# Performance work log

Hardware: AMD Instinct MI355X
Metric: run time of the kernel (lower is better)

## Reference

```python
import jax, jax.numpy as jnp
import numpy as np

HID = 100  # LSTM hidden size (fixed in module)


def _lstm_final(x, Wih, Whh, bih, bhh, reverse):
    # x: [N, T, Hin]; returns final hidden state [N, HID] (PyTorch gate order i,f,g,o)
    xs = jnp.flip(x, axis=1) if reverse else x
    pre = jnp.einsum('nth,gh->ntg', xs, Wih) + bih + bhh  # [N, T, 4*HID]
    N = x.shape[0]
    h0 = jnp.zeros((N, HID), x.dtype)
    c0 = jnp.zeros((N, HID), x.dtype)

    def step(carry, pt):
        h, c = carry
        g = pt + h @ Whh.T
        i, f, gg, o = jnp.split(g, 4, axis=-1)
        c = jax.nn.sigmoid(f) * c + jax.nn.sigmoid(i) * jnp.tanh(gg)
        h = jax.nn.sigmoid(o) * jnp.tanh(c)
        return (h, c), None

    (h, c), _ = jax.lax.scan(step, (h0, c0), jnp.swapaxes(pre, 0, 1))
    return h


def setup_inputs():
    key = jax.random.key(0)
    ks = jax.random.split(key, 16)
    H, B, S, NP, PL = 768, 40, 128, 100, 20
    w = lambda k, shape: jax.random.normal(k, shape, jnp.float32) * 0.02
    return {
        'bert_output': jax.random.normal(ks[0], (B, S, H), jnp.float32),
        'commonsense': jax.random.normal(ks[1], (B * NP, PL, H), jnp.float32),
        'attention_mask': jnp.ones((B, S), jnp.int32),
        'commonsense_mask': jnp.ones((B, NP), jnp.int32),
        'b_size': 8, 'num_cand': 5, 'num_path': NP, 'path_len': PL,
        'lstm_Wih_f': w(ks[2], (4 * HID, H)), 'lstm_Whh_f': w(ks[3], (4 * HID, HID)),
        'lstm_bih_f': jnp.zeros((4 * HID,), jnp.float32), 'lstm_bhh_f': jnp.zeros((4 * HID,), jnp.float32),
        'lstm_Wih_b': w(ks[4], (4 * HID, H)), 'lstm_Whh_b': w(ks[5], (4 * HID, HID)),
        'lstm_bih_b': jnp.zeros((4 * HID,), jnp.float32), 'lstm_bhh_b': jnp.zeros((4 * HID,), jnp.float32),
        'proj_W': w(ks[6], (H, 2 * HID)), 'proj_b': jnp.zeros((H,), jnp.float32),
        'W1_w': w(ks[7], (1, H)), 'W1_b': jnp.zeros((1,), jnp.float32),
        'W2_w': w(ks[8], (1, H)), 'W2_b': jnp.zeros((1,), jnp.float32),
        'W3': w(ks[9], (1, 1, H)),
        'attp_W': w(ks[10], (H, 4 * H)), 'attp_b': jnp.zeros((H,), jnp.float32),
        'ln_w': jnp.ones((H,), jnp.float32), 'ln_b': jnp.zeros((H,), jnp.float32),
    }


def reference(bert_output, commonsense, attention_mask, commonsense_mask,
              b_size, num_cand, num_path, path_len,
              lstm_Wih_f, lstm_Whh_f, lstm_bih_f, lstm_bhh_f,
              lstm_Wih_b, lstm_Whh_b, lstm_bih_b, lstm_bhh_b,
              proj_W, proj_b, W1_w, W1_b, W2_w, W2_b, W3,
              attp_W, attp_b, ln_w, ln_b):
    Bc = b_size * num_cand
    # bidirectional LSTM over commonsense paths; only final hidden states are used
    h_f = _lstm_final(commonsense, lstm_Wih_f, lstm_Whh_f, lstm_bih_f, lstm_bhh_f, False)
    h_b = _lstm_final(commonsense, lstm_Wih_b, lstm_Whh_b, lstm_bih_b, lstm_bhh_b, True)
    enc = jnp.concatenate([h_f, h_b], axis=-1)               # [Bc*NP, 200]
    cs = jax.nn.relu(enc @ proj_W.T + proj_b).reshape(Bc, num_path, -1)  # [B, P, H]
    # trilinear BiDAF-style scores
    part1 = bert_output @ W1_w.T + W1_b                      # [B, S, 1]
    part2 = (cs @ W2_w.T + W2_b).transpose(0, 2, 1)          # [B, 1, P]
    part3 = jnp.einsum('bsh,bph->bsp', W3 * bert_output, cs)  # [B, S, P]
    mask_cs = (1.0 - commonsense_mask.astype(jnp.float32)) * -10000.0
    mask_dqa = (1.0 - attention_mask.astype(jnp.float32)) * -10000.0
    total = part1 + part2 + part3 + mask_cs[:, None, :] + mask_dqa[:, :, None]
    cs_att = jax.nn.softmax(total, axis=-1)                  # over paths
    weight_cs = jnp.einsum('bsp,bph->bsh', cs_att, cs)
    ctx_att = jax.nn.softmax(total, axis=1)                  # over context tokens
    probs = jnp.einsum('bsp,btp->bst', cs_att, ctx_att)      # [B, S, S]
    weighted_context = jnp.einsum('bst,bth->bsh', probs, bert_output)
    cat = jnp.concatenate([bert_output, weight_cs, bert_output * weight_cs,
                           bert_output * weighted_context], axis=-1)
    x = jax.nn.relu(cat @ attp_W.T + attp_b) + bert_output
    u = x.mean(-1, keepdims=True)
    s = ((x - u) ** 2).mean(-1, keepdims=True)
    return ln_w * ((x - u) / jnp.sqrt(s + 1e-12)) + ln_b
```

## Files before the change

### kernel.cpp

```cpp
#include <hip/hip_runtime.h>


typedef unsigned short ushort_t;
typedef unsigned int u32;
typedef __attribute__((ext_vector_type(8))) short short8;
typedef __attribute__((ext_vector_type(4))) float f32x4;
typedef __attribute__((address_space(1))) const u32 gu32;
typedef __attribute__((address_space(3))) u32 lu32;

__device__ __forceinline__ ushort_t f2bf(float f) {
  u32 x = __builtin_bit_cast(u32, f);
  u32 r = (x + 0x7fffu + ((x >> 16) & 1u)) >> 16;
  return (ushort_t)r;
}
__device__ __forceinline__ float bflo(u32 u) { return __builtin_bit_cast(float, u << 16); }
__device__ __forceinline__ float bfhi(u32 u) { return __builtin_bit_cast(float, u & 0xffff0000u); }
__device__ __forceinline__ u32 cvtpk(float lo, float hi) {
  u32 r;
  asm("v_cvt_pk_bf16_f32 %0, %1, %2" : "=v"(r) : "v"(lo), "v"(hi));
  return r;
}

__device__ __forceinline__ float sigm(float x) { return 1.f / (1.f + __expf(-x)); }
__device__ __forceinline__ float tanh_f(float x) { return 1.f - 2.f / (__expf(2.f * x) + 1.f); }


__global__ void prep_weights(const float* __restrict__ Wih_f, const float* __restrict__ Wih_b,
                             const float* __restrict__ Whh_f, const float* __restrict__ Whh_b,
                             const float* __restrict__ bih_f, const float* __restrict__ bhh_f,
                             const float* __restrict__ bih_b, const float* __restrict__ bhh_b,
                             const float* __restrict__ projW, const float* __restrict__ attpW,
                             ushort_t* __restrict__ wihcat, ushort_t* __restrict__ whhcat,
                             float* __restrict__ biascat, ushort_t* __restrict__ projw_bf,
                             ushort_t* __restrict__ attpw_bf) {
  const int TOT = 614400 + 102400 + 800 + 196608 + 2359296;
  for (int idx = blockIdx.x * 256 + threadIdx.x; idx < TOT; idx += gridDim.x * 256) {
    if (idx < 614400) {
      int g = idx / 768, k = idx % 768;
      float v = g < 400 ? Wih_f[g * 768 + k] : Wih_b[(g - 400) * 768 + k];
      wihcat[idx] = f2bf(v);
    } else if (idx < 716800) {
      int e = idx - 614400; int g = e / 128, j = e % 128;
      float v = 0.f;
      if (j < 100) v = g < 400 ? Whh_f[g * 100 + j] : Whh_b[(g - 400) * 100 + j];
      whhcat[e] = f2bf(v);
    } else if (idx < 717600) {
      int g = idx - 716800;
      biascat[g] = g < 400 ? bih_f[g] + bhh_f[g] : bih_b[g - 400] + bhh_b[g - 400];
    } else if (idx < 914208) {
      int e = idx - 717600; int o = e / 256, j = e % 256;
      float v = 0.f;
      if (j < 100) v = projW[o * 200 + j];
      else if (j >= 128 && j < 228) v = projW[o * 200 + 100 + (j - 128)];
      projw_bf[e] = f2bf(v);
    } else {
      int e = idx - 914208;
      attpw_bf[e] = f2bf(attpW[e]);
    }
  }
}

__global__ void convert_x_t(const float4* __restrict__ x4, ushort_t* __restrict__ xb) {
  for (int i = blockIdx.x * 256 + threadIdx.x; i < 15360000; i += gridDim.x * 256) {
    int seq = i / 3840;
    int rem = i - seq * 3840;
    int t = rem / 192;
    int k4 = rem - t * 192;
    float4 v = x4[i];
    ushort4 o;
    o.x = f2bf(v.x); o.y = f2bf(v.y); o.z = f2bf(v.z); o.w = f2bf(v.w);
    *reinterpret_cast<ushort4*>(&xb[((size_t)t * 4000 + seq) * 768 + k4 * 4]) = o;
  }
}

__global__ __launch_bounds__(256) void prep_bert(const float* __restrict__ bert,
                                                 const float* __restrict__ W3,
                                                 ushort_t* __restrict__ bw3,
                                                 ushort_t* __restrict__ bT) {
  __shared__ ushort_t tl[64 * 130];
  int ht = blockIdx.x, b = blockIdx.y;
  int h0 = ht * 64, tid = threadIdx.x;
  for (int e = tid; e < 8192; e += 256) {
    int t = e >> 6, hh = e & 63;
    float v = bert[((size_t)b * 128 + t) * 768 + h0 + hh];
    bw3[((size_t)b * 128 + t) * 768 + h0 + hh] = f2bf(v * W3[h0 + hh]);
    tl[hh * 130 + t] = f2bf(v);
  }
  __syncthreads();
  for (int e = tid; e < 8192; e += 256) {
    int hh = e >> 7, t = e & 127;
    bT[((size_t)b * 768 + h0 + hh) * 128 + t] = tl[hh * 130 + t];
  }
}

__global__ __launch_bounds__(256) void csT_k(const ushort_t* __restrict__ csb,
                                             ushort_t* __restrict__ csT) {
  __shared__ ushort_t tl[64 * 130];
  int ht = blockIdx.x, b = blockIdx.y;
  int h0 = ht * 64, tid = threadIdx.x;
  for (int e = tid; e < 6400; e += 256) {
    int p = e >> 6, hh = e & 63;
    tl[hh * 130 + p] = csb[((size_t)b * 100 + p) * 768 + h0 + hh];
  }
  __syncthreads();
  for (int e = tid; e < 8192; e += 256) {
    int hh = e >> 7, p = e & 127;
    csT[((size_t)b * 768 + h0 + hh) * 128 + p] = (p < 100) ? tl[hh * 130 + p] : (ushort_t)0;
  }
}


template <int EPI>
__global__ __launch_bounds__(256) void gemm128(
    const ushort_t* __restrict__ A, int lda,
    const ushort_t* __restrict__ B, int ldb,
    int M, int N, int KT,
    const float* __restrict__ bias,
    const float* __restrict__ resid,
    float* __restrict__ C, int ldc,
    ushort_t* __restrict__ C2,
    int nbn, int swq, int swr)
{
  __shared__ __align__(16) ushort_t lsA[128 * 64];
  __shared__ __align__(16) ushort_t lsB[128 * 64];
  int bm, bn;
  if (nbn > 0) {
    int bid = blockIdx.x, xcd = bid & 7, slot = bid >> 3;
    int L = (xcd < swr) ? xcd * (swq + 1) + slot
                        : swr * (swq + 1) + (xcd - swr) * swq + slot;
    bm = L / nbn; bn = L - bm * nbn;
  } else {
    bm = blockIdx.x; bn = blockIdx.y;
  }
  int m0 = bm * 128, n0 = bn * 128;
  int tid = threadIdx.x, lane = tid & 63, w = tid >> 6;
  int wr = w >> 1, wc = w & 1;
  int l15 = lane & 15, lk = lane >> 4;
  f32x4 acc[4][4];
  #pragma unroll
  for (int i = 0; i < 4; ++i)
    #pragma unroll
    for (int j = 0; j < 4; ++j)
      #pragma unroll
      for (int r = 0; r < 4; ++r) acc[i][j][r] = 0.f;

  int r_in = lane >> 3, p = lane & 7;
  for (int kt = 0; kt < KT; ++kt) {
    __syncthreads();
    #pragma unroll
    for (int i = 0; i < 4; ++i) {
      int seg = w * 4 + i;
      int row = seg * 8 + r_in;
      int sl = p ^ (row & 7);
      int m = m0 + row;
      if (m < M)
        __builtin_amdgcn_global_load_lds(
            (gu32*)(A + (size_t)m * lda + kt * 64 + sl * 8),
            (lu32*)(lsA + seg * 512), 16, 0, 0);
      int n = n0 + row;
      if (n < N)
        __builtin_amdgcn_global_load_lds(
            (gu32*)(B + (size_t)n * ldb + kt * 64 + sl * 8),
            (lu32*)(lsB + seg * 512), 16, 0, 0);
    }
    __syncthreads();
    #pragma unroll
    for (int ks = 0; ks < 2; ++ks) {
      short8 af[4], bfv[4];
      #pragma unroll
      for (int f = 0; f < 4; ++f) {
        int row = wr * 64 + f * 16 + l15;
        af[f] = *reinterpret_cast<const short8*>(
            &lsA[row * 64 + (((ks * 4 + lk) ^ (row & 7)) << 3)]);
        int rowb = wc * 64 + f * 16 + l15;
        bfv[f] = *reinterpret_cast<const short8*>(
            &lsB[rowb * 64 + (((ks * 4 + lk) ^ (rowb & 7)) << 3)]);
      }
      #pragma unroll
      for (int fm = 0; fm < 4; ++fm)
        #pragma unroll
        for (int fn = 0; fn < 4; ++fn)
          acc[fm][fn] = __builtin_amdgcn_mfma_f32_16x16x32_bf16(af[fm], bfv[fn], acc[fm][fn], 0, 0, 0);
    }
  }
  if (EPI == 0) {
    ushort_t* P = (ushort_t*)C;
    #pragma unroll
    for (int fm = 0; fm < 4; ++fm) {
      int mb = m0 + wr * 64 + fm * 16;
      int t = mb / 4000;
      int sq = mb - t * 4000;
      int cch = sq >> 4;
      #pragma unroll
      for (int fn = 0; fn < 4; ++fn) {
        int nb = n0 + wc * 64 + fn * 16;
        if (nb < N) {
          int nl = nb < 400 ? nb : nb - 400;
          int nq = (nb < 400 ? 0 : 25) + (nl >> 4);
          float bsv = bias[nb + l15];
          uint2 pk;
          pk.x = cvtpk(acc[fm][fn][0] + bsv, acc[fm][fn][1] + bsv);
          pk.y = cvtpk(acc[fm][fn][2] + bsv, acc[fm][fn][3] + bsv);
          *reinterpret_cast<uint2*>(
              &P[((((size_t)t * 250 + cch) * 50 + nq) << 8) + l15 * 16 + lk * 4]) = pk;
        }
      }
    }
  } else {
    #pragma unroll
    for (int fm = 0; fm < 4; ++fm)
      #pragma unroll
      for (int fn = 0; fn < 4; ++fn)
        #pragma unroll
        for (int r = 0; r < 4; ++r) {
          int m = m0 + wr * 64 + fm * 16 + lk * 4 + r;
          int n = n0 + wc * 64 + fn * 16 + l15;
          if (m < M && n < N) {
            float v = acc[fm][fn][r] + bias[n];
            v = fmaxf(v, 0.f);
            if (EPI == 2) v += resid[(size_t)m * ldc + n];
            C[(size_t)m * ldc + n] = v;
            if (EPI == 1 && C2) C2[(size_t)m * ldc + n] = f2bf(v);
          }
        }
  }
}


template <int EPI>
__global__ __launch_bounds__(256) void gemm128b(
    const ushort_t* __restrict__ A, long long sA, int lda,
    const ushort_t* __restrict__ Bm, long long sB, int ldb,
    int M, int N, int KT,
    float* __restrict__ Cf, ushort_t* __restrict__ Cb, long long sC, int ldc,
    const float* __restrict__ p1, const float* __restrict__ p2,
    const int* __restrict__ am, const int* __restrict__ cm)
{
  __shared__ __align__(16) ushort_t lsA[128 * 64];
  __shared__ __align__(16) ushort_t lsB[128 * 64];
  int b = blockIdx.z;
  const ushort_t* Ab = A + (size_t)b * sA;
  const ushort_t* Bb = Bm + (size_t)b * sB;
  int n0 = blockIdx.x * 128;
  int tid = threadIdx.x, lane = tid & 63, w = tid >> 6;
  int wr = w >> 1, wc = w & 1;
  int l15 = lane & 15, lk = lane >> 4;
  f32x4 acc[4][4];
  #pragma unroll
  for (int i = 0; i < 4; ++i)
    #pragma unroll
    for (int j = 0; j < 4; ++j)
      #pragma unroll
      for (int r = 0; r < 4; ++r) acc[i][j][r] = 0.f;

  int r_in = lane >> 3, p = lane & 7;
  for (int kt = 0; kt < KT; ++kt) {
    __syncthreads();
    #pragma unroll
    for (int i = 0; i < 4; ++i) {
      int seg = w * 4 + i;
      int row = seg * 8 + r_in;
      int sl = p ^ (row & 7);
      if (row < M)
        __builtin_amdgcn_global_load_lds(
            (gu32*)(Ab + (size_t)row * lda + kt * 64 + sl * 8),
            (lu32*)(lsA + seg * 512), 16, 0, 0);
      int n = n0 + row;
      if (n < N)
        __builtin_amdgcn_global_load_lds(
            (gu32*)(Bb + (size_t)n * ldb + kt * 64 + sl * 8),
            (lu32*)(lsB + seg * 512), 16, 0, 0);
    }
    __syncthreads();
    #pragma unroll
    for (int ks = 0; ks < 2; ++ks) {
      short8 af[4], bfv[4];
      #pragma unroll
      for (int f = 0; f < 4; ++f) {
        int row = wr * 64 + f * 16 + l15;
        af[f] = *reinterpret_cast<const short8*>(
            &lsA[row * 64 + (((ks * 4 + lk) ^ (row & 7)) << 3)]);
        int rowb = wc * 64 + f * 16 + l15;
        bfv[f] = *reinterpret_cast<const short8*>(
            &lsB[rowb * 64 + (((ks * 4 + lk) ^ (rowb & 7)) << 3)]);
      }
      #pragma unroll
      for (int fm = 0; fm < 4; ++fm)
        #pragma unroll
        for (int fn = 0; fn < 4; ++fn)
          acc[fm][fn] = __builtin_amdgcn_mfma_f32_16x16x32_bf16(af[fm], bfv[fn], acc[fm][fn], 0, 0, 0);
    }
  }
  #pragma unroll
  for (int fm = 0; fm < 4; ++fm)
    #pragma unroll
    for (int fn = 0; fn < 4; ++fn)
      #pragma unroll
      for (int r = 0; r < 4; ++r) {
        int m = wr * 64 + fm * 16 + lk * 4 + r;
        int n = n0 + wc * 64 + fn * 16 + l15;
        if (m < M && n < N) {
          float v = acc[fm][fn][r];
          if (EPI == 10) {
            v += p1[b * M + m] + p2[b * N + n];
            v += (1.f - (float)am[b * M + m]) * -10000.f;
            v += (1.f - (float)cm[b * N + n]) * -10000.f;
            Cf[(size_t)b * sC + (size_t)m * ldc + n] = v;
          } else {
            Cb[(size_t)b * sC + (size_t)m * ldc + n] = f2bf(v);
          }
        }
      }
}


__global__ __launch_bounds__(256) void lstm_recur(
    const ushort_t* __restrict__ pre,
    const ushort_t* __restrict__ whh,
    ushort_t* __restrict__ hcat)
{
  __shared__ __align__(16) ushort_t gx[25 * 256];
  __shared__ __align__(16) ushort_t h_lds[16 * 128];

  int dir = blockIdx.y;
  int c = blockIdx.x;
  int tid = threadIdx.x, lane = tid & 63, w = tid >> 6;
  int s = lane & 15, lk = lane >> 4;

  short8 wf[7][4];
  #pragma unroll
  for (int qi = 0; qi < 7; ++qi) {
    int q = w + qi * 4;
    if (q < 25) {
      const ushort_t* wp = whh + ((size_t)dir * 400 + q * 16 + s) * 128;
      #pragma unroll
      for (int ks = 0; ks < 4; ++ks)
        wf[qi][ks] = *reinterpret_cast<const short8*>(wp + ks * 32 + lk * 8);
    }
  }
  for (int e = tid; e < 1024; e += 256)
    *reinterpret_cast<u32*>(&h_lds[e * 2]) = 0u;

  float cst[2][4];
  #pragma unroll
  for (int g = 0; g < 2; ++g)
    #pragma unroll
    for (int r = 0; r < 4; ++r) cst[g][r] = 0.f;

  uint2 pvA[7], pvB[7];
  {
    int tt0 = dir ? 19 : 0;
    const ushort_t* pb = pre + ((((size_t)tt0 * 250 + c) * 50 + dir * 25) << 8);
    #pragma unroll
    for (int qi = 0; qi < 7; ++qi) {
      int q = w + qi * 4;
      if (q < 25) pvA[qi] = *reinterpret_cast<const uint2*>(pb + (q << 8) + s * 16 + lk * 4);
    }
  }
  __syncthreads();

  auto step = [&](uint2 (&pvc)[7], uint2 (&pvn)[7], int t) {
    f32x4 acc[7];
    #pragma unroll
    for (int qi = 0; qi < 7; ++qi)
      #pragma unroll
      for (int r = 0; r < 4; ++r) acc[qi][r] = 0.f;
    #pragma unroll
    for (int ks = 0; ks < 4; ++ks) {
      short8 af = *reinterpret_cast<const short8*>(
          &h_lds[s * 128 + (((ks * 4 + lk) ^ s) << 3)]);
      #pragma unroll
      for (int qi = 0; qi < 7; ++qi)
        if (w + qi * 4 < 25)
          acc[qi] = __builtin_amdgcn_mfma_f32_16x16x32_bf16(af, wf[qi][ks], acc[qi], 0, 0, 0);
    }
    #pragma unroll
    for (int qi = 0; qi < 7; ++qi)
      if (w + qi * 4 < 25) {
        acc[qi][0] += bflo(pvc[qi].x); acc[qi][1] += bfhi(pvc[qi].x);
        acc[qi][2] += bflo(pvc[qi].y); acc[qi][3] += bfhi(pvc[qi].y);
      }
    if (t + 1 < 20) {
      int tn = dir ? 19 - (t + 1) : (t + 1);
      const ushort_t* pb = pre + ((((size_t)tn * 250 + c) * 50 + dir * 25) << 8);
      #pragma unroll
      for (int qi = 0; qi < 7; ++qi) {
        int q = w + qi * 4;
        if (q < 25) pvn[qi] = *reinterpret_cast<const uint2*>(pb + (q << 8) + s * 16 + lk * 4);
      }
    }
    #pragma unroll
    for (int qi = 0; qi < 7; ++qi) {
      int q = w + qi * 4;
      if (q < 25) {
        ushort4 pk;
        pk.x = f2bf(acc[qi][0]); pk.y = f2bf(acc[qi][1]);
        pk.z = f2bf(acc[qi][2]); pk.w = f2bf(acc[qi][3]);
        *reinterpret_cast<ushort4*>(&gx[(q << 8) + s * 16 + lk * 4]) = pk;
      }
    }
    __syncthreads();
    #pragma unroll
    for (int gd = 0; gd < 2; ++gd) {
      int gi = w + gd * 4;
      if (gi < 7) {
        int j = gi * 16 + s;
        if (j < 100) {
          auto ld2 = [&](int q, int sp) {
            return *reinterpret_cast<const uint2*>(&gx[(q << 8) + sp * 16 + lk * 4]);
          };
          uint2 iv = ld2(gi, s);
          uint2 fv = (s < 12) ? ld2(6 + gi, s + 4) : ld2(7 + gi, s - 12);
          uint2 gv = (s < 8) ? ld2(12 + gi, s + 8) : ld2(13 + gi, s - 8);
          uint2 ov = (s < 4) ? ld2(18 + gi, s + 12) : ld2(19 + gi, s - 4);
          float ia[4] = {bflo(iv.x), bfhi(iv.x), bflo(iv.y), bfhi(iv.y)};
          float fa[4] = {bflo(fv.x), bfhi(fv.x), bflo(fv.y), bfhi(fv.y)};
          float ga[4] = {bflo(gv.x), bfhi(gv.x), bflo(gv.y), bfhi(gv.y)};
          float oa[4] = {bflo(ov.x), bfhi(ov.x), bflo(ov.y), bfhi(ov.y)};
          #pragma unroll
          for (int r = 0; r < 4; ++r) {
            float cc = sigm(fa[r]) * cst[gd][r] + sigm(ia[r]) * tanh_f(ga[r]);
            cst[gd][r] = cc;
            int row = lk * 4 + r;
            h_lds[row * 128 + (((j >> 3) ^ row) << 3) + (j & 7)] =
                f2bf(sigm(oa[r]) * tanh_f(cc));
          }
        }
      }
    }
    __syncthreads();
  };

  #pragma unroll 1
  for (int tp = 0; tp < 10; ++tp) {
    step(pvA, pvB, 2 * tp);
    step(pvB, pvA, 2 * tp + 1);
  }

  {
    int row = tid >> 4, sl = tid & 15;
    uint2 v = *reinterpret_cast<const uint2*>(&h_lds[row * 128 + ((sl ^ row) << 3)]);
    *reinterpret_cast<uint2*>(&hcat[(size_t)(c * 16 + row) * 256 + dir * 128 + sl * 8]) = v;
  }
}


__global__ void rowdot(const float* __restrict__ X, int ld, const float* __restrict__ w,
                       const float* __restrict__ b0, float* __restrict__ out, int nrows) {
  int row = blockIdx.x;
  if (row >= nrows) return;
  int lane = threadIdx.x;
  const float* x = X + (size_t)row * ld;
  float s = 0.f;
  for (int k = lane; k < 768; k += 64) s += x[k] * w[k];
  for (int off = 32; off; off >>= 1) s += __shfl_down(s, off);
  if (lane == 0) out[row] = s + b0[0];
}

__global__ void softmax_both(const float* __restrict__ total,
                             ushort_t* __restrict__ csatt,
                             ushort_t* __restrict__ ctxatt) {
  int bid = blockIdx.x;
  int lane = threadIdx.x;
  if (bid < 5120) {
    const float* x = total + (size_t)bid * 100;
    float e0 = x[lane];
    bool has1 = (lane + 64) < 100;
    float e1 = has1 ? x[lane + 64] : -3.4e38f;
    float m = fmaxf(e0, e1);
    for (int off = 32; off; off >>= 1) m = fmaxf(m, __shfl_xor(m, off));
    float s0 = expf(e0 - m), s1 = has1 ? expf(e1 - m) : 0.f;
    float s = s0 + s1;
    for (int off = 32; off; off >>= 1) s += __shfl_xor(s, off);
    float inv = 1.f / s;
    csatt[(size_t)bid * 128 + lane] = f2bf(s0 * inv);
    csatt[(size_t)bid * 128 + lane + 64] = has1 ? f2bf(s1 * inv) : (ushort_t)0;
  } else {
    int idx = bid - 5120;
    int b = idx / 100, p = idx - b * 100;
    const float* base = total + (size_t)b * 12800 + p;
    float e0 = base[lane * 100], e1 = base[(lane + 64) * 100];
    float m = fmaxf(e0, e1);
    for (int off = 32; off; off >>= 1) m = fmaxf(m, __shfl_xor(m, off));
    float s0 = expf(e0 - m), s1 = expf(e1 - m);
    float s = s0 + s1;
    for (int off = 32; off; off >>= 1) s += __shfl_xor(s, off);
    float inv = 1.f / s;
    ctxatt[((size_t)b * 128 + lane) * 128 + p] = f2bf(s0 * inv);
    ctxatt[((size_t)b * 128 + lane + 64) * 128 + p] = f2bf(s1 * inv);
  }
}

__global__ void catk(const float* __restrict__ bert, const ushort_t* __restrict__ wcs,
                     const ushort_t* __restrict__ wctx, ushort_t* __restrict__ cat) {
  const int TOT = 5120 * 3072;
  for (int i = blockIdx.x * 256 + threadIdx.x; i < TOT; i += gridDim.x * 256) {
    int row = i / 3072, col = i - row * 3072;
    int seg = col / 768;
    int h = col - seg * 768;
    size_t e = (size_t)row * 768 + h;
    ushort_t o;
    if (seg == 0) o = f2bf(bert[e]);
    else if (seg == 1) o = wcs[e];
    else if (seg == 2) o = f2bf(bert[e] * bflo((u32)wcs[e]));
    else o = f2bf(bert[e] * bflo((u32)wctx[e]));
    cat[i] = o;
  }
}

__global__ __launch_bounds__(256) void layernorm(float* __restrict__ X,
                                                 const float* __restrict__ w,
                                                 const float* __restrict__ bta) {
  int row = blockIdx.x;
  float* x = X + (size_t)row * 768;
  int t = threadIdx.x;
  float v[3];
  float s = 0.f;
  #pragma unroll
  for (int i = 0; i < 3; ++i) { v[i] = x[t + 256 * i]; s += v[i]; }
  __shared__ float red[256];
  red[t] = s; __syncthreads();
  for (int off = 128; off; off >>= 1) { if (t < off) red[t] += red[t + off]; __syncthreads(); }
  float mean = red[0] * (1.f / 768.f);
  __syncthreads();
  float q = 0.f;
  #pragma unroll
  for (int i = 0; i < 3; ++i) { float d = v[i] - mean; q += d * d; }
  red[t] = q; __syncthreads();
  for (int off = 128; off; off >>= 1) { if (t < off) red[t] += red[t + off]; __syncthreads(); }
  float inv = rsqrtf(red[0] * (1.f / 768.f) + 1e-12f);
  #pragma unroll
  for (int i = 0; i < 3; ++i) {
    int k = t + 256 * i;
    x[k] = w[k] * ((v[i] - mean) * inv) + bta[k];
  }
}


extern "C" void kernel_launch(void* const* d_in, const int* in_sizes, int n_in,
                              void* d_out, int out_size, void* d_ws, size_t ws_size,
                              hipStream_t stream) {
  (void)in_sizes; (void)n_in; (void)out_size; (void)ws_size;
  const float* bert  = (const float*)d_in[0];
  const float* cmn   = (const float*)d_in[1];
  const int*   amask = (const int*)d_in[2];
  const int*   cmask = (const int*)d_in[3];
  const float* Wih_f = (const float*)d_in[8];
  const float* Whh_f = (const float*)d_in[9];
  const float* bih_f = (const float*)d_in[10];
  const float* bhh_f = (const float*)d_in[11];
  const float* Wih_b = (const float*)d_in[12];
  const float* Whh_b = (const float*)d_in[13];
  const float* bih_b = (const float*)d_in[14];
  const float* bhh_b = (const float*)d_in[15];
  const float* projW = (const float*)d_in[16];
  const float* projb = (const float*)d_in[17];
  const float* W1w   = (const float*)d_in[18];
  const float* W1b   = (const float*)d_in[19];
  const float* W2w   = (const float*)d_in[20];
  const float* W2b   = (const float*)d_in[21];
  const float* W3    = (const float*)d_in[22];
  const float* attpW = (const float*)d_in[23];
  const float* attpb = (const float*)d_in[24];
  const float* lnw   = (const float*)d_in[25];
  const float* lnb   = (const float*)d_in[26];

  char* base = (char*)d_ws;
  size_t off = 0;
  auto alloc = [&](size_t bytes) -> char* {
    char* r = base + off;
    off += (bytes + 255) & ~(size_t)255;
    return r;
  };
  ushort_t* wihcat   = (ushort_t*)alloc(800 * 768 * 2);
  ushort_t* whhcat   = (ushort_t*)alloc(800 * 128 * 2);
  float*    biascat  = (float*)alloc(800 * 4);
  ushort_t* projw_bf = (ushort_t*)alloc(768 * 256 * 2);
  ushort_t* attpw_bf = (ushort_t*)alloc(768 * 3072 * 2);
  ushort_t* hcat     = (ushort_t*)alloc(4000 * 256 * 2);
  float*    cs       = (float*)alloc((size_t)4000 * 768 * 4);
  ushort_t* cs_bf    = (ushort_t*)alloc((size_t)4000 * 768 * 2);
  ushort_t* csT      = (ushort_t*)alloc((size_t)40 * 768 * 128 * 2);
  float*    part1    = (float*)alloc(5120 * 4);
  float*    part2    = (float*)alloc(4000 * 4);
  float*    total_s  = (float*)alloc((size_t)40 * 128 * 100 * 4);
  ushort_t* csatt_bf = (ushort_t*)alloc((size_t)40 * 128 * 128 * 2);
  ushort_t* ctxatt_bf= (ushort_t*)alloc((size_t)40 * 128 * 128 * 2);
  ushort_t* probs_bf = (ushort_t*)alloc((size_t)40 * 128 * 128 * 2);
  ushort_t* wcs_bf   = (ushort_t*)alloc((size_t)40 * 128 * 768 * 2);
  ushort_t* wctx_bf  = (ushort_t*)alloc((size_t)40 * 128 * 768 * 2);
  ushort_t* bw3_bf   = (ushort_t*)alloc((size_t)40 * 128 * 768 * 2);
  ushort_t* bertT    = (ushort_t*)alloc((size_t)40 * 768 * 128 * 2);
  ushort_t* cat      = (ushort_t*)alloc((size_t)5120 * 3072 * 2);
  ushort_t* x_bf     = (ushort_t*)alloc((size_t)20 * 4000 * 768 * 2);
  ushort_t* pre      = (ushort_t*)alloc((size_t)20 * 250 * 50 * 256 * 2);

  prep_weights<<<512, 256, 0, stream>>>(Wih_f, Wih_b, Whh_f, Whh_b, bih_f, bhh_f, bih_b, bhh_b,
                                        projW, attpW, wihcat, whhcat, biascat, projw_bf, attpw_bf);
  prep_bert<<<dim3(12, 40), 256, 0, stream>>>(bert, W3, bw3_bf, bertT);
  convert_x_t<<<2048, 256, 0, stream>>>((const float4*)cmn, x_bf);

  gemm128<0><<<4375, 256, 0, stream>>>(x_bf, 768, wihcat, 768, 80000, 800, 12,
                                       biascat, nullptr, (float*)pre, 0, nullptr, 7, 546, 7);
  lstm_recur<<<dim3(250, 2), 256, 0, stream>>>(pre, whhcat, hcat);

  gemm128<1><<<dim3(32, 6), 256, 0, stream>>>(hcat, 256, projw_bf, 256, 4000, 768, 4,
                                              projb, nullptr, cs, 768, cs_bf, 0, 0, 0);
  csT_k<<<dim3(12, 40), 256, 0, stream>>>(cs_bf, csT);
  rowdot<<<5120, 64, 0, stream>>>(bert, 768, W1w, W1b, part1, 5120);
  rowdot<<<4000, 64, 0, stream>>>(cs, 768, W2w, W2b, part2, 4000);

  gemm128b<10><<<dim3(1, 1, 40), 256, 0, stream>>>(
      bw3_bf, 98304LL, 768, cs_bf, 76800LL, 768, 128, 100, 12,
      total_s, nullptr, 12800LL, 100, part1, part2, amask, cmask);
  softmax_both<<<9120, 64, 0, stream>>>(total_s, csatt_bf, ctxatt_bf);
  gemm128b<11><<<dim3(6, 1, 40), 256, 0, stream>>>(
      csatt_bf, 16384LL, 128, csT, 98304LL, 128, 128, 768, 2,
      nullptr, wcs_bf, 98304LL, 768, nullptr, nullptr, nullptr, nullptr);
  gemm128b<11><<<dim3(1, 1, 40), 256, 0, stream>>>(
      csatt_bf, 16384LL, 128, ctxatt_bf, 16384LL, 128, 128, 128, 2,
      nullptr, probs_bf, 16384LL, 128, nullptr, nullptr, nullptr, nullptr);
  gemm128b<11><<<dim3(6, 1, 40), 256, 0, stream>>>(
      probs_bf, 16384LL, 128, bertT, 98304LL, 128, 128, 768, 2,
      nullptr, wctx_bf, 98304LL, 768, nullptr, nullptr, nullptr, nullptr);

  catk<<<2048, 256, 0, stream>>>(bert, wcs_bf, wctx_bf, cat);
  gemm128<2><<<240, 256, 0, stream>>>(cat, 3072, attpw_bf, 3072, 5120, 768, 48,
                                      attpb, bert, (float*)d_out, 768, nullptr, 6, 30, 0);
  layernorm<<<5120, 256, 0, stream>>>((float*)d_out, lnw, lnb);
}
```

Baseline: 534.6 us.

## Fuse fp32-to-bf16 input conversion into LSTM input GEMM, merge rowdots, vectorize concat

```diff
diff --git a/kernel.cpp b/kernel.cpp
--- a/kernel.cpp
+++ b/kernel.cpp
@@ -60,19 +60,6 @@
   }
 }
 
-__global__ void convert_x_t(const float4* __restrict__ x4, ushort_t* __restrict__ xb) {
-  for (int i = blockIdx.x * 256 + threadIdx.x; i < 15360000; i += gridDim.x * 256) {
-    int seq = i / 3840;
-    int rem = i - seq * 3840;
-    int t = rem / 192;
-    int k4 = rem - t * 192;
-    float4 v = x4[i];
-    ushort4 o;
-    o.x = f2bf(v.x); o.y = f2bf(v.y); o.z = f2bf(v.z); o.w = f2bf(v.w);
-    *reinterpret_cast<ushort4*>(&xb[((size_t)t * 4000 + seq) * 768 + k4 * 4]) = o;
-  }
-}
-
 __global__ __launch_bounds__(256) void prep_bert(const float* __restrict__ bert,
                                                  const float* __restrict__ W3,
                                                  ushort_t* __restrict__ bw3,
@@ -106,6 +93,114 @@
   for (int e = tid; e < 8192; e += 256) {
     int hh = e >> 7, p = e & 127;
     csT[((size_t)b * 768 + h0 + hh) * 128 + p] = (p < 100) ? tl[hh * 130 + p] : (ushort_t)0;
+  }
+}
+
+
+__global__ __launch_bounds__(256) void gemm_pre_f(
+    const float* __restrict__ X,
+    const ushort_t* __restrict__ B,
+    const float* __restrict__ bias,
+    ushort_t* __restrict__ P)
+{
+  __shared__ __align__(16) float lsA[128 * 64];
+  __shared__ __align__(16) ushort_t lsB[128 * 64];
+  int bid = blockIdx.x;
+  int xcd = bid & 7, slot = bid >> 3;
+  int L = (xcd < 7) ? xcd * 547 + slot : 3829 + slot;
+  int bm = L / 7, bn = L - bm * 7;
+  int m0 = bm * 128, n0 = bn * 128;
+  int tid = threadIdx.x, lane = tid & 63, w = tid >> 6;
+  int wr = w >> 1, wc = w & 1;
+  int l15 = lane & 15, lk = lane >> 4;
+  f32x4 acc[4][4];
+  #pragma unroll
+  for (int i = 0; i < 4; ++i)
+    #pragma unroll
+    for (int j = 0; j < 4; ++j)
+      #pragma unroll
+      for (int r = 0; r < 4; ++r) acc[i][j][r] = 0.f;
+
+  size_t abase[8];
+  #pragma unroll
+  for (int i = 0; i < 8; ++i) {
+    int seg = w * 8 + i;
+    int row = seg * 4 + (lane >> 4);
+    int m = m0 + row;
+    int t = m / 4000, sq = m - t * 4000;
+    int lc = (lane & 15) ^ (row & 15);
+    abase[i] = ((size_t)sq * 20 + t) * 768 + lc * 4;
+  }
+  int r_in = lane >> 3, pslot = lane & 7;
+
+  for (int kt = 0; kt < 12; ++kt) {
+    __syncthreads();
+    #pragma unroll
+    for (int i = 0; i < 8; ++i) {
+      int seg = w * 8 + i;
+      __builtin_amdgcn_global_load_lds(
+          (gu32*)(X + abase[i] + kt * 64),
+          (lu32*)((char*)lsA + seg * 1024), 16, 0, 0);
+    }
+    #pragma unroll
+    for (int i = 0; i < 4; ++i) {
+      int seg = w * 4 + i;
+      int row = seg * 8 + r_in;
+      int sl = pslot ^ (row & 7);
+      int n = n0 + row;
+      if (n < 800)
+        __builtin_amdgcn_global_load_lds(
+            (gu32*)(B + (size_t)n * 768 + kt * 64 + sl * 8),
+            (lu32*)(lsB + seg * 512), 16, 0, 0);
+    }
+    __syncthreads();
+    #pragma unroll
+    for (int ks = 0; ks < 2; ++ks) {
+      short8 af[4], bfv[4];
+      #pragma unroll
+      for (int f = 0; f < 4; ++f) {
+        int row = wr * 64 + f * 16 + l15;
+        int c0 = ks * 8 + lk * 2;
+        int pc0 = c0 ^ (row & 15), pc1 = (c0 + 1) ^ (row & 15);
+        float4 v0 = *reinterpret_cast<const float4*>(&lsA[row * 64 + pc0 * 4]);
+        float4 v1 = *reinterpret_cast<const float4*>(&lsA[row * 64 + pc1 * 4]);
+        int4 pk;
+        pk.x = (int)cvtpk(v0.x, v0.y);
+        pk.y = (int)cvtpk(v0.z, v0.w);
+        pk.z = (int)cvtpk(v1.x, v1.y);
+        pk.w = (int)cvtpk(v1.z, v1.w);
+        af[f] = __builtin_bit_cast(short8, pk);
+        int rowb = wc * 64 + f * 16 + l15;
+        bfv[f] = *reinterpret_cast<const short8*>(
+            &lsB[rowb * 64 + (((ks * 4 + lk) ^ (rowb & 7)) << 3)]);
+      }
+      #pragma unroll
+      for (int fm = 0; fm < 4; ++fm)
+        #pragma unroll
+        for (int fn = 0; fn < 4; ++fn)
+          acc[fm][fn] = __builtin_amdgcn_mfma_f32_16x16x32_bf16(af[fm], bfv[fn], acc[fm][fn], 0, 0, 0);
+    }
+  }
+  #pragma unroll
+  for (int fm = 0; fm < 4; ++fm) {
+    int mb = m0 + wr * 64 + fm * 16;
+    int t = mb / 4000;
+    int sq = mb - t * 4000;
+    int cch = sq >> 4;
+    #pragma unroll
+    for (int fn = 0; fn < 4; ++fn) {
+      int nb = n0 + wc * 64 + fn * 16;
+      if (nb < 800) {
+        int nl = nb < 400 ? nb : nb - 400;
+        int nq = (nb < 400 ? 0 : 25) + (nl >> 4);
+        float bsv = bias[nb + l15];
+        uint2 pk;
+        pk.x = cvtpk(acc[fm][fn][0] + bsv, acc[fm][fn][1] + bsv);
+        pk.y = cvtpk(acc[fm][fn][2] + bsv, acc[fm][fn][3] + bsv);
+        *reinterpret_cast<uint2*>(
+            &P[((((size_t)t * 250 + cch) * 50 + nq) << 8) + l15 * 16 + lk * 4]) = pk;
+      }
+    }
   }
 }
 
@@ -183,47 +278,22 @@
           acc[fm][fn] = __builtin_amdgcn_mfma_f32_16x16x32_bf16(af[fm], bfv[fn], acc[fm][fn], 0, 0, 0);
     }
   }
-  if (EPI == 0) {
-    ushort_t* P = (ushort_t*)C;
-    #pragma unroll
-    for (int fm = 0; fm < 4; ++fm) {
-      int mb = m0 + wr * 64 + fm * 16;
-      int t = mb / 4000;
-      int sq = mb - t * 4000;
-      int cch = sq >> 4;
-      #pragma unroll
-      for (int fn = 0; fn < 4; ++fn) {
-        int nb = n0 + wc * 64 + fn * 16;
-        if (nb < N) {
-          int nl = nb < 400 ? nb : nb - 400;
-          int nq = (nb < 400 ? 0 : 25) + (nl >> 4);
-          float bsv = bias[nb + l15];
-          uint2 pk;
-          pk.x = cvtpk(acc[fm][fn][0] + bsv, acc[fm][fn][1] + bsv);
-          pk.y = cvtpk(acc[fm][fn][2] + bsv, acc[fm][fn][3] + bsv);
-          *reinterpret_cast<uint2*>(
-              &P[((((size_t)t * 250 + cch) * 50 + nq) << 8) + l15 * 16 + lk * 4]) = pk;
+  #pragma unroll
+  for (int fm = 0; fm < 4; ++fm)
+    #pragma unroll
+    for (int fn = 0; fn < 4; ++fn)
+      #pragma unroll
+      for (int r = 0; r < 4; ++r) {
+        int m = m0 + wr * 64 + fm * 16 + lk * 4 + r;
+        int n = n0 + wc * 64 + fn * 16 + l15;
+        if (m < M && n < N) {
+          float v = acc[fm][fn][r] + bias[n];
+          v = fmaxf(v, 0.f);
+          if (EPI == 2) v += resid[(size_t)m * ldc + n];
+          C[(size_t)m * ldc + n] = v;
+          if (EPI == 1 && C2) C2[(size_t)m * ldc + n] = f2bf(v);
         }
       }
-    }
-  } else {
-    #pragma unroll
-    for (int fm = 0; fm < 4; ++fm)
-      #pragma unroll
-      for (int fn = 0; fn < 4; ++fn)
-        #pragma unroll
-        for (int r = 0; r < 4; ++r) {
-          int m = m0 + wr * 64 + fm * 16 + lk * 4 + r;
-          int n = n0 + wc * 64 + fn * 16 + l15;
-          if (m < M && n < N) {
-            float v = acc[fm][fn][r] + bias[n];
-            v = fmaxf(v, 0.f);
-            if (EPI == 2) v += resid[(size_t)m * ldc + n];
-            C[(size_t)m * ldc + n] = v;
-            if (EPI == 1 && C2) C2[(size_t)m * ldc + n] = f2bf(v);
-          }
-        }
-  }
 }
 
 
@@ -445,16 +515,22 @@
 }
 
 
-__global__ void rowdot(const float* __restrict__ X, int ld, const float* __restrict__ w,
-                       const float* __restrict__ b0, float* __restrict__ out, int nrows) {
+__global__ void rowdot2(const float* __restrict__ bert, const float* __restrict__ cs,
+                        const float* __restrict__ W1w, const float* __restrict__ W1b,
+                        const float* __restrict__ W2w, const float* __restrict__ W2b,
+                        float* __restrict__ part1, float* __restrict__ part2) {
   int row = blockIdx.x;
-  if (row >= nrows) return;
   int lane = threadIdx.x;
-  const float* x = X + (size_t)row * ld;
+  const float* x;
+  const float* wv;
+  float b0;
+  float* out;
+  if (row < 5120) { x = bert + (size_t)row * 768; wv = W1w; b0 = W1b[0]; out = part1 + row; }
+  else { int r = row - 5120; x = cs + (size_t)r * 768; wv = W2w; b0 = W2b[0]; out = part2 + r; }
   float s = 0.f;
-  for (int k = lane; k < 768; k += 64) s += x[k] * w[k];
+  for (int k = lane; k < 768; k += 64) s += x[k] * wv[k];
   for (int off = 32; off; off >>= 1) s += __shfl_down(s, off);
-  if (lane == 0) out[row] = s + b0[0];
+  if (lane == 0) *out = s + b0;
 }
 
 __global__ void softmax_both(const float* __restrict__ total,
@@ -493,18 +569,24 @@
 
 __global__ void catk(const float* __restrict__ bert, const ushort_t* __restrict__ wcs,
                      const ushort_t* __restrict__ wctx, ushort_t* __restrict__ cat) {
-  const int TOT = 5120 * 3072;
+  const int TOT = 5120 * 192;
   for (int i = blockIdx.x * 256 + threadIdx.x; i < TOT; i += gridDim.x * 256) {
-    int row = i / 3072, col = i - row * 3072;
-    int seg = col / 768;
-    int h = col - seg * 768;
-    size_t e = (size_t)row * 768 + h;
-    ushort_t o;
-    if (seg == 0) o = f2bf(bert[e]);
-    else if (seg == 1) o = wcs[e];
-    else if (seg == 2) o = f2bf(bert[e] * bflo((u32)wcs[e]));
-    else o = f2bf(bert[e] * bflo((u32)wctx[e]));
-    cat[i] = o;
+    int row = i / 192, h4 = i - row * 192;
+    size_t e = (size_t)row * 768 + h4 * 4;
+    float4 bv = *reinterpret_cast<const float4*>(bert + e);
+    ushort4 wv = *reinterpret_cast<const ushort4*>(wcs + e);
+    ushort4 cv = *reinterpret_cast<const ushort4*>(wctx + e);
+    ushort_t* out = cat + (size_t)row * 3072 + h4 * 4;
+    ushort4 s0, s2, s3;
+    s0.x = f2bf(bv.x); s0.y = f2bf(bv.y); s0.z = f2bf(bv.z); s0.w = f2bf(bv.w);
+    s2.x = f2bf(bv.x * bflo((u32)wv.x)); s2.y = f2bf(bv.y * bflo((u32)wv.y));
+    s2.z = f2bf(bv.z * bflo((u32)wv.z)); s2.w = f2bf(bv.w * bflo((u32)wv.w));
+    s3.x = f2bf(bv.x * bflo((u32)cv.x)); s3.y = f2bf(bv.y * bflo((u32)cv.y));
+    s3.z = f2bf(bv.z * bflo((u32)cv.z)); s3.w = f2bf(bv.w * bflo((u32)cv.w));
+    *reinterpret_cast<ushort4*>(out) = s0;
+    *reinterpret_cast<ushort4*>(out + 768) = wv;
+    *reinterpret_cast<ushort4*>(out + 1536) = s2;
+    *reinterpret_cast<ushort4*>(out + 2304) = s3;
   }
 }
 
@@ -592,23 +674,19 @@
   ushort_t* bw3_bf   = (ushort_t*)alloc((size_t)40 * 128 * 768 * 2);
   ushort_t* bertT    = (ushort_t*)alloc((size_t)40 * 768 * 128 * 2);
   ushort_t* cat      = (ushort_t*)alloc((size_t)5120 * 3072 * 2);
-  ushort_t* x_bf     = (ushort_t*)alloc((size_t)20 * 4000 * 768 * 2);
   ushort_t* pre      = (ushort_t*)alloc((size_t)20 * 250 * 50 * 256 * 2);
 
   prep_weights<<<512, 256, 0, stream>>>(Wih_f, Wih_b, Whh_f, Whh_b, bih_f, bhh_f, bih_b, bhh_b,
                                         projW, attpW, wihcat, whhcat, biascat, projw_bf, attpw_bf);
   prep_bert<<<dim3(12, 40), 256, 0, stream>>>(bert, W3, bw3_bf, bertT);
-  convert_x_t<<<2048, 256, 0, stream>>>((const float4*)cmn, x_bf);
-
-  gemm128<0><<<4375, 256, 0, stream>>>(x_bf, 768, wihcat, 768, 80000, 800, 12,
-                                       biascat, nullptr, (float*)pre, 0, nullptr, 7, 546, 7);
+
+  gemm_pre_f<<<4375, 256, 0, stream>>>(cmn, wihcat, biascat, pre);
   lstm_recur<<<dim3(250, 2), 256, 0, stream>>>(pre, whhcat, hcat);
 
   gemm128<1><<<dim3(32, 6), 256, 0, stream>>>(hcat, 256, projw_bf, 256, 4000, 768, 4,
                                               projb, nullptr, cs, 768, cs_bf, 0, 0, 0);
   csT_k<<<dim3(12, 40), 256, 0, stream>>>(cs_bf, csT);
-  rowdot<<<5120, 64, 0, stream>>>(bert, 768, W1w, W1b, part1, 5120);
-  rowdot<<<4000, 64, 0, stream>>>(cs, 768, W2w, W2b, part2, 4000);
+  rowdot2<<<9120, 64, 0, stream>>>(bert, cs, W1w, W1b, W2w, W2b, part1, part2);
 
   gemm128b<10><<<dim3(1, 1, 40), 256, 0, stream>>>(
       bw3_bf, 98304LL, 768, cs_bf, 76800LL, 768, 128, 100, 12,
```

Result: no change. 535.4 us (+0.2%).
